# Performance work log

Measured on AMD Instinct MI355X. Metric: run time of the kernel, lower is better.

The kernel has to match this reference:

```python
import jax, jax.numpy as jnp
import numpy as np
import math

B, T, N, D = 8, 12, 500, 512  # batch, time(heads), nodes, K*d
FACTOR = 5
SAMPLE_K = min(FACTOR * math.ceil(math.log(N)), N)  # = 35, also n_top (N_Q == N_K)
W_SCALE = 0.02


def setup_inputs() -> dict:
    key = jax.random.key(0)
    ks = jax.random.split(key, 9)
    f32 = jnp.float32
    return {
        "X":   jax.random.normal(ks[0], (B, T, N, D), f32),
        "STE": jax.random.normal(ks[1], (B, T, N, D), f32),
        "Wq":  jax.random.normal(ks[2], (2 * D, D), f32) * W_SCALE,
        "bq":  jnp.zeros((D,), f32),
        "Wk":  jax.random.normal(ks[3], (2 * D, D), f32) * W_SCALE,
        "bk":  jnp.zeros((D,), f32),
        "Wv":  jax.random.normal(ks[4], (2 * D, D), f32) * W_SCALE,
        "bv":  jnp.zeros((D,), f32),
        "sample_idx": jax.random.randint(ks[5], (N, SAMPLE_K), 0, N, jnp.int32),
    }


def reference(X, STE, Wq, bq, Wk, bk, Wv, bv, sample_idx):
    # concat spatial features with spatio-temporal embedding -> projections
    Xc = jnp.concatenate([X, STE], axis=-1)                  # [B,T,N,2D]
    q = jax.nn.relu(Xc @ Wq + bq)                            # [B,T,N,D]
    k = jax.nn.relu(Xc @ Wk + bk)
    v = jax.nn.relu(Xc @ Wv + bv)

    n_top = SAMPLE_K
    # _prob_QK: sampled Q-K scores. Since SAMPLE_K*D >> N, computing the full
    # [B,T,N,N] score matrix and gathering the sampled columns is strictly
    # cheaper in memory than materializing K_sample [B,T,N,S,D] as torch does;
    # the math (Q_K_sample values) is identical.
    scores_full = jnp.einsum('bhld,bhmd->bhlm', q, k)        # [B,T,N,N]
    QK_sample = jnp.take_along_axis(
        scores_full, sample_idx[None, None, :, :], axis=3)   # [B,T,N,S]
    # sparsity measure M = max - mean (mean over L_K = N)
    M = QK_sample.max(axis=-1) - QK_sample.sum(axis=-1) / N  # [B,T,N]
    _, idx = jax.lax.top_k(M, n_top)                         # [B,T,n_top]

    # reduced-query full attention scores (gather rows of full scores == Q_reduce @ K^T)
    scores = jnp.take_along_axis(scores_full, idx[..., None], axis=2)  # [B,T,u,N]
    scores = scores * (1.0 / math.sqrt(D))

    # ProbMask (mask_flag=True): causal mask per selected query position
    j = jnp.arange(N)
    mask = j[None, None, None, :] > idx[..., None]           # [B,T,u,N]
    scores = jnp.where(mask, -jnp.inf, scores)
    attn = jax.nn.softmax(scores, axis=-1)                   # [B,T,u,N]
    ctx_new = jnp.einsum('bhun,bhnd->bhud', attn, v)         # [B,T,u,D]

    # initial context = causal cumsum of V, then scatter-update selected queries
    context = jnp.cumsum(v, axis=2)                          # [B,T,N,D]
    bi = jnp.arange(B)[:, None, None]
    hi = jnp.arange(T)[None, :, None]
    context = context.at[bi, hi, idx].set(ctx_new)
    # .transpose(2,1) in torch -> swap axes 1 and 2
    return context.transpose(0, 2, 1, 3)                     # [B,N,T,D]
```

## Files before the change

### kernel.cpp

```cpp
#include <hip/hip_runtime.h>
#include <math.h>

#define B_    8
#define T_    12
#define BT    96
#define NN    500
#define DD    512
#define KK    1024
#define SK    35
#define MROWS 48000

typedef __bf16 bf16x8 __attribute__((ext_vector_type(8)));
typedef float f32x4 __attribute__((ext_vector_type(4)));
typedef unsigned short u16;
typedef unsigned int u32;
typedef u16 ushort8_t __attribute__((ext_vector_type(8)));
typedef u16 ushort4_t __attribute__((ext_vector_type(4)));

__device__ __forceinline__ u16 bf_hi(float x) {
  __bf16 h = (__bf16)x;
  return __builtin_bit_cast(u16, h);
}
__device__ __forceinline__ float bf_tof(u16 b) {
  unsigned int u = ((unsigned int)b) << 16;
  return __builtin_bit_cast(float, u);
}

__device__ __forceinline__ int lds_off(int row, int kq) {
  return row * 32 + ((kq ^ ((row >> 1) & 3)) * 8);
}

__device__ __forceinline__ void gload_lds16(const u16* g, u16* l) {
  __builtin_amdgcn_global_load_lds(
      (const __attribute__((address_space(1))) u32*)g,
      (__attribute__((address_space(3))) u32*)l, 16, 0, 0);
}

__global__ __launch_bounds__(256) void convW_kernel(
    const float* __restrict__ W, u16* __restrict__ Bth, u16* __restrict__ Btl)
{
  const int n = blockIdx.x;
  const int k0 = threadIdx.x * 4;
  float xs[4];
#pragma unroll
  for (int j = 0; j < 4; ++j) xs[j] = W[(size_t)(k0 + j) * 512 + n];
  ushort4_t hi, lo;
#pragma unroll
  for (int j = 0; j < 4; ++j) {
    u16 h = bf_hi(xs[j]);
    hi[j] = h;
    lo[j] = bf_hi(xs[j] - bf_tof(h));
  }
  *(ushort4_t*)(Bth + (size_t)n * 1024 + k0) = hi;
  *(ushort4_t*)(Btl + (size_t)n * 1024 + k0) = lo;
}

template<int PASSES>
__global__ __launch_bounds__(256) void mfma_proj(
    const float* __restrict__ X, const float* __restrict__ STE,
    const u16* __restrict__ Bth, const u16* __restrict__ Btl,
    const float* __restrict__ bias, float* __restrict__ out)
{
  constexpr int NT = (PASSES == 3) ? 4 : 2;
  __shared__ u16 ldsbuf[2 * NT * 4096];
  const int tid = threadIdx.x;
  const int lane = tid & 63;
  const int wid = tid >> 6;
  const int wm = wid >> 1, wn = wid & 1;
  const int orig = blockIdx.x;
  const int xcd = orig & 7, pos = orig >> 3;
  const int wg = (xcd < 4 ? xcd * 188 : 752 + (xcd - 4) * 187) + pos;
  const int r0 = (wg >> 2) * 128;
  const int c0 = (wg & 3) * 128;
  const int fr = lane & 15, fk = lane >> 4;
  const int rin = lane >> 2;
  const int qq  = lane & 3;

  f32x4 acc[4][4];
#pragma unroll
  for (int m = 0; m < 4; ++m)
#pragma unroll
    for (int n = 0; n < 4; ++n) acc[m][n] = f32x4{0.f, 0.f, 0.f, 0.f};

  float4 a0[2], a1[2];

  auto LOAD_A = [&](int kt) {
    const int kk0 = kt * 32;
#pragma unroll
    for (int p = 0; p < 2; ++p) {
      const int c = tid + p * 256;
      const int row = c >> 2, kc = c & 3;
      const int col = kk0 + kc * 8;
      const float* src = (col < 512)
          ? (X + (size_t)(r0 + row) * 512 + col)
          : (STE + (size_t)(r0 + row) * 512 + (col - 512));
      a0[p] = *(const float4*)src;
      a1[p] = *(const float4*)(src + 4);
    }
  };
  auto ISSUE_B = [&](int buf, int kt) {
    u16* bBh = ldsbuf + buf * NT * 4096 + 4096;
    u16* bBl = ldsbuf + buf * NT * 4096 + 12288;
    const int kk0 = kt * 32;
#pragma unroll
    for (int i = 0; i < 2; ++i) {
      const int ch = wid * 2 + i;
      const int row = ch * 16 + rin;
      const int kq = qq ^ ((row >> 1) & 3);
      const size_t gb = (size_t)(c0 + row) * 1024 + kk0 + kq * 8;
      gload_lds16(Bth + gb, bBh + ch * 512);
      if (PASSES == 3) gload_lds16(Btl + gb, bBl + ch * 512);
    }
  };
  auto WRITE_A = [&](int buf) {
    u16* bAh = ldsbuf + buf * NT * 4096;
    u16* bAl = bAh + 8192;
#pragma unroll
    for (int p = 0; p < 2; ++p) {
      const int c = tid + p * 256;
      const int row = c >> 2, kc = c & 3;
      const int dst = lds_off(row, kc);
      float xs[8] = {a0[p].x, a0[p].y, a0[p].z, a0[p].w,
                     a1[p].x, a1[p].y, a1[p].z, a1[p].w};
      ushort8_t hi, lo;
#pragma unroll
      for (int j = 0; j < 8; ++j) {
        u16 h = bf_hi(xs[j]);
        hi[j] = h;
        if (PASSES == 3) lo[j] = bf_hi(xs[j] - bf_tof(h));
      }
      *(ushort8_t*)&bAh[dst] = hi;
      if (PASSES == 3) *(ushort8_t*)&bAl[dst] = lo;
    }
  };

  LOAD_A(0);
  ISSUE_B(0, 0);
  WRITE_A(0);
  __syncthreads();
  int cur = 0;

  for (int kt = 0; kt < 32; ++kt) {
    const bool more = (kt + 1 < 32);
    if (more) {
      LOAD_A(kt + 1);
      ISSUE_B(cur ^ 1, kt + 1);
    }
    u16* bAh = ldsbuf + cur * NT * 4096;
    u16* bBh = bAh + 4096;
    u16* bAl = bAh + 8192;
    u16* bBl = bAh + 12288;
    bf16x8 ah[4], al[4];
#pragma unroll
    for (int m = 0; m < 4; ++m) {
      const int off = lds_off(wm * 64 + m * 16 + fr, fk);
      ah[m] = *(const bf16x8*)&bAh[off];
      if (PASSES == 3) al[m] = *(const bf16x8*)&bAl[off];
    }
#pragma unroll
    for (int n = 0; n < 4; ++n) {
      const int off = lds_off(wn * 64 + n * 16 + fr, fk);
      bf16x8 bh = *(const bf16x8*)&bBh[off];
      bf16x8 bl;
      if (PASSES == 3) bl = *(const bf16x8*)&bBl[off];
#pragma unroll
      for (int m = 0; m < 4; ++m) {
        acc[m][n] = __builtin_amdgcn_mfma_f32_16x16x32_bf16(
            ah[m], bh, acc[m][n], 0, 0, 0);
        if (PASSES == 3) {
          acc[m][n] = __builtin_amdgcn_mfma_f32_16x16x32_bf16(
              ah[m], bl, acc[m][n], 0, 0, 0);
          acc[m][n] = __builtin_amdgcn_mfma_f32_16x16x32_bf16(
              al[m], bh, acc[m][n], 0, 0, 0);
        }
      }
    }
    if (more) WRITE_A(cur ^ 1);
    __syncthreads();
    cur ^= 1;
  }

#pragma unroll
  for (int n = 0; n < 4; ++n) {
    const int col = c0 + wn * 64 + n * 16 + fr;
    const float bb = bias[col];
#pragma unroll
    for (int m = 0; m < 4; ++m) {
      const int rowb = r0 + wm * 64 + m * 16 + fk * 4;
#pragma unroll
      for (int r = 0; r < 4; ++r)
        out[(size_t)(rowb + r) * 512 + col] = fmaxf(acc[m][n][r] + bb, 0.f);
    }
  }
}

__global__ __launch_bounds__(256) void sampled_M_kernel(
    const float* __restrict__ q, const float* __restrict__ k,
    const int* __restrict__ sidx, float* __restrict__ Mout)
{
  const int tid = threadIdx.x;
  const int lane = tid & 63, wid = tid >> 6;
  const int bid = blockIdx.x;
  const int xcd = bid & 7, j = bid >> 3;
  const int btg = j / 125, ub = j - btg * 125;
  const int bt = btg * 8 + xcd;
  __shared__ int sIdx[4][SK];
  if (tid < 4 * SK) {
    const int w = tid / SK, s = tid - w * SK;
    sIdx[w][s] = sidx[(ub * 4 + w) * SK + s];
  }
  __syncthreads();
  const int nn = ub * 4 + wid;
  const int n = bt * NN + nn;
  const float* qrow = q + (size_t)n * DD + lane * 8;
  float4 q0 = *(const float4*)qrow;
  float4 q1 = *(const float4*)(qrow + 4);
  const float* kbase = k + (size_t)bt * NN * DD + lane * 8;
  float mx = -INFINITY, sm = 0.f;
  for (int s0 = 0; s0 < SK; s0 += 5) {
    float p[5];
#pragma unroll
    for (int u = 0; u < 5; ++u) {
      const float* krow = kbase + (size_t)sIdx[wid][s0 + u] * DD;
      float4 k0 = *(const float4*)krow;
      float4 k1 = *(const float4*)(krow + 4);
      p[u] = q0.x*k0.x + q0.y*k0.y + q0.z*k0.z + q0.w*k0.w
           + q1.x*k1.x + q1.y*k1.y + q1.z*k1.z + q1.w*k1.w;
    }
#pragma unroll
    for (int off = 32; off > 0; off >>= 1)
#pragma unroll
      for (int u = 0; u < 5; ++u) p[u] += __shfl_xor(p[u], off);
#pragma unroll
    for (int u = 0; u < 5; ++u) { mx = fmaxf(mx, p[u]); sm += p[u]; }
  }
  if (lane == 0) Mout[n] = mx - sm * (1.0f / (float)NN);
}

__global__ __launch_bounds__(256) void topk_kernel(
    const float* __restrict__ Mb, int* __restrict__ idxb,
    int* __restrict__ sqi, int* __restrict__ su)
{
  const int bt = blockIdx.x;
  const int tid = threadIdx.x;
  __shared__ float mv[NN];
  __shared__ float rv[256];
  __shared__ int ri[256];
  __shared__ int qsel[SK];
  for (int n = tid; n < NN; n += 256) mv[n] = Mb[(size_t)bt * NN + n];
  __syncthreads();
  for (int it = 0; it < SK; ++it) {
    float bv = -INFINITY; int bi = NN;
    for (int n = tid; n < NN; n += 256) {
      float x = mv[n];
      if (x > bv) { bv = x; bi = n; }
    }
    rv[tid] = bv; ri[tid] = bi;
    __syncthreads();
    for (int sft = 128; sft > 0; sft >>= 1) {
      if (tid < sft) {
        float xv = rv[tid + sft]; int xi = ri[tid + sft];
        if (xv > rv[tid] || (xv == rv[tid] && xi < ri[tid])) {
          rv[tid] = xv; ri[tid] = xi;
        }
      }
      __syncthreads();
    }
    if (tid == 0) {
      idxb[bt * SK + it] = ri[0];
      qsel[it] = ri[0];
      mv[ri[0]] = -INFINITY;
    }
    __syncthreads();
  }
  if (tid < SK) {
    int myqi = qsel[tid];
    int rank = 0;
    for (int j = 0; j < SK; ++j) rank += (qsel[j] < myqi);
    sqi[bt * SK + rank] = myqi;
    su[bt * SK + rank] = tid;
  }
}

__global__ __launch_bounds__(256) void attn_part_kernel(
    const float* __restrict__ q, const float* __restrict__ k,
    const float* __restrict__ v, const int* __restrict__ sqi,
    float* __restrict__ pO, float* __restrict__ pm, float* __restrict__ pl)
{
  const int bid = blockIdx.x;
  const int xcd = bid & 7, j = bid >> 3;
  const int btg = j / 35, rem = j - btg * 35;
  const int g = rem / 5, c = rem % 5;
  const int bt = btg * 8 + xcd;
  const int base = bt * SK + g * 5;
  const int c0 = c * 100;
  const int tid = threadIdx.x;
  const int lane = tid & 63, wid = tid >> 6;

  __shared__ float sc[5][100];
  __shared__ int qg[5];
  __shared__ float pmx[5], psm[5];
  if (tid < 5) qg[tid] = sqi[base + tid];
  __syncthreads();
  const int gq = qg[4];
  const int mend = (gq < c0 + 99) ? gq : (c0 + 99);

  float4 qr[5][2];
#pragma unroll
  for (int jj = 0; jj < 5; ++jj) {
    const float* qp = q + ((size_t)bt * NN + qg[jj]) * DD + lane * 8;
    qr[jj][0] = *(const float4*)qp;
    qr[jj][1] = *(const float4*)(qp + 4);
  }
  const float scale = 0.044194173824159216f;

  for (int m = c0 + wid; m <= mend; m += 4) {
    const float* krow = k + ((size_t)bt * NN + m) * DD + lane * 8;
    float4 k0 = *(const float4*)krow;
    float4 k1 = *(const float4*)(krow + 4);
    float p[5];
#pragma unroll
    for (int jj = 0; jj < 5; ++jj) {
      p[jj] = qr[jj][0].x*k0.x + qr[jj][0].y*k0.y
            + qr[jj][0].z*k0.z + qr[jj][0].w*k0.w
            + qr[jj][1].x*k1.x + qr[jj][1].y*k1.y
            + qr[jj][1].z*k1.z + qr[jj][1].w*k1.w;
    }
#pragma unroll
    for (int off = 32; off > 0; off >>= 1)
#pragma unroll
      for (int jj = 0; jj < 5; ++jj) p[jj] += __shfl_xor(p[jj], off);
    if (lane == 0) {
#pragma unroll
      for (int jj = 0; jj < 5; ++jj) sc[jj][m - c0] = p[jj] * scale;
    }
  }
  __syncthreads();

  for (int jj = wid; jj < 5; jj += 4) {
    const int qe = (qg[jj] < c0 + 99) ? qg[jj] : (c0 + 99);
    const int len = qe - c0 + 1;
    float mx = -3e38f;
    for (int i = lane; i < len; i += 64) mx = fmaxf(mx, sc[jj][i]);
#pragma unroll
    for (int off = 32; off > 0; off >>= 1) mx = fmaxf(mx, __shfl_xor(mx, off));
    float sm = 0.f;
    for (int i = lane; i < len; i += 64) {
      float e = __expf(sc[jj][i] - mx);
      sc[jj][i] = e;
      sm += e;
    }
#pragma unroll
    for (int off = 32; off > 0; off >>= 1) sm += __shfl_xor(sm, off);
    if (lane == 0) { pmx[jj] = mx; psm[jj] = sm; }
  }
  __syncthreads();

  float a0[5] = {0.f,0.f,0.f,0.f,0.f}, a1[5] = {0.f,0.f,0.f,0.f,0.f};
  const float* vb = v + (size_t)bt * NN * DD;
  for (int m = c0; m <= mend; ++m) {
    float v0 = vb[(size_t)m * DD + tid];
    float v1 = vb[(size_t)m * DD + tid + 256];
#pragma unroll
    for (int jj = 0; jj < 5; ++jj) {
      if (m <= qg[jj]) {
        float w = sc[jj][m - c0];
        a0[jj] = fmaf(w, v0, a0[jj]);
        a1[jj] = fmaf(w, v1, a1[jj]);
      }
    }
  }

  const int pidx = (bt * 7 + g) * 5 + c;
  if (tid < 5) {
    pm[pidx * 5 + tid] = pmx[tid];
    pl[pidx * 5 + tid] = psm[tid];
  }
#pragma unroll
  for (int jj = 0; jj < 5; ++jj) {
    float* po = pO + ((size_t)(pidx * 5 + jj)) * DD;
    po[tid] = a0[jj];
    po[tid + 256] = a1[jj];
  }
}

__global__ __launch_bounds__(512) void attn_combine_kernel(
    const float* __restrict__ pO, const float* __restrict__ pm,
    const float* __restrict__ pl, const int* __restrict__ su,
    float* __restrict__ ctxn)
{
  const int bid = blockIdx.x;
  const int bt = bid / SK, s = bid % SK;
  const int g = s / 5, jj = s % 5;
  const int d = threadIdx.x;
  __shared__ float w[5];
  __shared__ float linv;
  if (d == 0) {
    float m_[5], l_[5], mx = -3e38f;
#pragma unroll
    for (int c = 0; c < 5; ++c) {
      const int pidx = (bt * 7 + g) * 5 + c;
      m_[c] = pm[pidx * 5 + jj];
      l_[c] = pl[pidx * 5 + jj];
      mx = fmaxf(mx, m_[c]);
    }
    float lt = 0.f;
#pragma unroll
    for (int c = 0; c < 5; ++c) {
      float wc = __expf(m_[c] - mx);
      w[c] = wc;
      lt += wc * l_[c];
    }
    linv = 1.f / lt;
  }
  __syncthreads();
  float o = 0.f;
#pragma unroll
  for (int c = 0; c < 5; ++c) {
    const int pidx = (bt * 7 + g) * 5 + c;
    o = fmaf(w[c], pO[((size_t)(pidx * 5 + jj)) * DD + d], o);
  }
  const int u = su[bt * SK + s];
  ctxn[((size_t)bt * SK + u) * DD + d] = o * linv;
}

__global__ __launch_bounds__(512) void vchunk_sum_kernel(
    const float* __restrict__ v, float* __restrict__ csum)
{
  const int ch = blockIdx.x, bt = blockIdx.y;
  const int d = threadIdx.x;
  const float* vb = v + ((size_t)bt * NN + ch * 50) * DD + d;
  float s = 0.f;
  for (int n = 0; n < 50; ++n) s += vb[(size_t)n * DD];
  csum[((size_t)bt * 10 + ch) * DD + d] = s;
}

__global__ __launch_bounds__(512) void cumsum_scatter2_kernel(
    const float* __restrict__ v, const int* __restrict__ idxb,
    const float* __restrict__ ctxn, const float* __restrict__ csum,
    float* __restrict__ out)
{
  const int ch = blockIdx.x, bt = blockIdx.y;
  const int b = bt / T_, t = bt % T_;
  const int d = threadIdx.x;
  const int n0 = ch * 50;
  __shared__ int sel[50];
  if (threadIdx.x < 50) sel[threadIdx.x] = -1;
  __syncthreads();
  if (threadIdx.x < SK) {
    int qi = idxb[bt * SK + threadIdx.x];
    if (qi >= n0 && qi < n0 + 50) sel[qi - n0] = threadIdx.x;
  }
  __syncthreads();
  float s = 0.f;
  for (int c = 0; c < ch; ++c) s += csum[((size_t)bt * 10 + c) * DD + d];
  for (int i = 0; i < 50; ++i) {
    s += v[((size_t)bt * NN + n0 + i) * DD + d];
    float o = s;
    int u = sel[i];
    if (u >= 0) o = ctxn[((size_t)bt * SK + u) * DD + d];
    out[(((size_t)b * NN + (n0 + i)) * T_ + t) * DD + d] = o;
  }
}

extern "C" void kernel_launch(void* const* d_in, const int* in_sizes, int n_in,
                              void* d_out, int out_size, void* d_ws, size_t ws_size,
                              hipStream_t stream) {
  const float* X   = (const float*)d_in[0];
  const float* STE = (const float*)d_in[1];
  const float* Wq  = (const float*)d_in[2];
  const float* bq  = (const float*)d_in[3];
  const float* Wk  = (const float*)d_in[4];
  const float* bk  = (const float*)d_in[5];
  const float* Wv  = (const float*)d_in[6];
  const float* bv  = (const float*)d_in[7];
  const int* sidx  = (const int*)d_in[8];
  float* out = (float*)d_out;

  float* q    = (float*)d_ws;
  float* k    = q + (size_t)MROWS * DD;
  float* v    = k + (size_t)MROWS * DD;
  float* Mb   = v + (size_t)MROWS * DD;
  int*   idxb = (int*)(Mb + MROWS);
  float* ctxn = (float*)(idxb + BT * SK);
  u16* Bqh = (u16*)(ctxn + (size_t)BT * SK * DD);
  u16* Bql = Bqh + (size_t)512 * 1024;
  u16* Bkh = Bql + (size_t)512 * 1024;
  u16* Bkl = Bkh + (size_t)512 * 1024;
  u16* Bvh = Bkl + (size_t)512 * 1024;
  u16* Bvl = Bvh + (size_t)512 * 1024;
  float* csum = (float*)Bqh;
  int*   sqi  = (int*)Bkh;
  int*   su   = sqi + BT * SK;
  float* pm   = (float*)(su + BT * SK);
  float* pl   = pm + 3360 * 5;
  float* pO   = (float*)d_out;
  (void)ws_size; (void)in_sizes; (void)n_in; (void)out_size;

  convW_kernel<<<512, 256, 0, stream>>>(Wq, Bqh, Bql);
  convW_kernel<<<512, 256, 0, stream>>>(Wk, Bkh, Bkl);
  convW_kernel<<<512, 256, 0, stream>>>(Wv, Bvh, Bvl);

  mfma_proj<3><<<1500, 256, 0, stream>>>(X, STE, Bqh, Bql, bq, q);
  mfma_proj<3><<<1500, 256, 0, stream>>>(X, STE, Bkh, Bkl, bk, k);
  mfma_proj<1><<<1500, 256, 0, stream>>>(X, STE, Bvh, Bvl, bv, v);

  sampled_M_kernel<<<12000, 256, 0, stream>>>(q, k, sidx, Mb);
  topk_kernel<<<BT, 256, 0, stream>>>(Mb, idxb, sqi, su);
  attn_part_kernel<<<3360, 256, 0, stream>>>(q, k, v, sqi, pO, pm, pl);
  attn_combine_kernel<<<3360, 512, 0, stream>>>(pO, pm, pl, su, ctxn);
  dim3 g5(10, BT);
  vchunk_sum_kernel<<<g5, 512, 0, stream>>>(v, csum);
  cumsum_scatter2_kernel<<<g5, 512, 0, stream>>>(v, idxb, ctxn, csum, out);
}
```

Baseline: 899.7 us.

## Load projection B operand directly from global into registers, bypassing LDS

The projection GEMM no longer stages the bf16 weight tiles (hi/lo) in shared memory through global_load_lds. Each wave now loads its B fragments straight from global memory into registers, double-buffered in registers, with the k-loop unrolled by two. This halves LDS usage and removes the LDS reads for B. In exchange it costs more VGPRs, and the B loads are redundant across the two wm waves and less coalesced, relying on L2/L1 hits.

```diff
diff --git a/kernel.cpp b/kernel.cpp
--- a/kernel.cpp
+++ b/kernel.cpp
@@ -30,12 +30,6 @@
   return row * 32 + ((kq ^ ((row >> 1) & 3)) * 8);
 }
 
-__device__ __forceinline__ void gload_lds16(const u16* g, u16* l) {
-  __builtin_amdgcn_global_load_lds(
-      (const __attribute__((address_space(1))) u32*)g,
-      (__attribute__((address_space(3))) u32*)l, 16, 0, 0);
-}
-
 __global__ __launch_bounds__(256) void convW_kernel(
     const float* __restrict__ W, u16* __restrict__ Bth, u16* __restrict__ Btl)
 {
@@ -61,8 +55,8 @@
     const u16* __restrict__ Bth, const u16* __restrict__ Btl,
     const float* __restrict__ bias, float* __restrict__ out)
 {
-  constexpr int NT = (PASSES == 3) ? 4 : 2;
-  __shared__ u16 ldsbuf[2 * NT * 4096];
+  constexpr int NA = (PASSES == 3) ? 2 : 1;
+  __shared__ u16 ldsA[2 * NA * 4096];
   const int tid = threadIdx.x;
   const int lane = tid & 63;
   const int wid = tid >> 6;
@@ -73,8 +67,6 @@
   const int r0 = (wg >> 2) * 128;
   const int c0 = (wg & 3) * 128;
   const int fr = lane & 15, fk = lane >> 4;
-  const int rin = lane >> 2;
-  const int qq  = lane & 3;
 
   f32x4 acc[4][4];
 #pragma unroll
@@ -82,7 +74,11 @@
 #pragma unroll
     for (int n = 0; n < 4; ++n) acc[m][n] = f32x4{0.f, 0.f, 0.f, 0.f};
 
+  const size_t bfo = (size_t)(c0 + wn * 64 + fr) * 1024 + fk * 8;
+
   float4 a0[2], a1[2];
+  bf16x8 bh0[4], bl0[4];
+  bf16x8 bh1[4], bl1[4];
 
   auto LOAD_A = [&](int kt) {
     const int kk0 = kt * 32;
@@ -98,23 +94,18 @@
       a1[p] = *(const float4*)(src + 4);
     }
   };
-  auto ISSUE_B = [&](int buf, int kt) {
-    u16* bBh = ldsbuf + buf * NT * 4096 + 4096;
-    u16* bBl = ldsbuf + buf * NT * 4096 + 12288;
-    const int kk0 = kt * 32;
-#pragma unroll
-    for (int i = 0; i < 2; ++i) {
-      const int ch = wid * 2 + i;
-      const int row = ch * 16 + rin;
-      const int kq = qq ^ ((row >> 1) & 3);
-      const size_t gb = (size_t)(c0 + row) * 1024 + kk0 + kq * 8;
-      gload_lds16(Bth + gb, bBh + ch * 512);
-      if (PASSES == 3) gload_lds16(Btl + gb, bBl + ch * 512);
+  auto LOAD_B = [&](int kt, bf16x8 (&h)[4], bf16x8 (&l)[4]) {
+    const int kk = kt * 32;
+#pragma unroll
+    for (int n = 0; n < 4; ++n) {
+      const size_t go = bfo + (size_t)n * 16384 + kk;
+      h[n] = *(const bf16x8*)(Bth + go);
+      if (PASSES == 3) l[n] = *(const bf16x8*)(Btl + go);
     }
   };
   auto WRITE_A = [&](int buf) {
-    u16* bAh = ldsbuf + buf * NT * 4096;
-    u16* bAl = bAh + 8192;
+    u16* bAh = ldsA + buf * NA * 4096;
+    u16* bAl = bAh + 4096;
 #pragma unroll
     for (int p = 0; p < 2; ++p) {
       const int c = tid + p * 256;
@@ -133,23 +124,9 @@
       if (PASSES == 3) *(ushort8_t*)&bAl[dst] = lo;
     }
   };
-
-  LOAD_A(0);
-  ISSUE_B(0, 0);
-  WRITE_A(0);
-  __syncthreads();
-  int cur = 0;
-
-  for (int kt = 0; kt < 32; ++kt) {
-    const bool more = (kt + 1 < 32);
-    if (more) {
-      LOAD_A(kt + 1);
-      ISSUE_B(cur ^ 1, kt + 1);
-    }
-    u16* bAh = ldsbuf + cur * NT * 4096;
-    u16* bBh = bAh + 4096;
-    u16* bAl = bAh + 8192;
-    u16* bBl = bAh + 12288;
+  auto COMPUTE = [&](int buf, const bf16x8 (&bh)[4], const bf16x8 (&bl)[4]) {
+    const u16* bAh = ldsA + buf * NA * 4096;
+    const u16* bAl = bAh + 4096;
     bf16x8 ah[4], al[4];
 #pragma unroll
     for (int m = 0; m < 4; ++m) {
@@ -158,26 +135,38 @@
       if (PASSES == 3) al[m] = *(const bf16x8*)&bAl[off];
     }
 #pragma unroll
-    for (int n = 0; n < 4; ++n) {
-      const int off = lds_off(wn * 64 + n * 16 + fr, fk);
-      bf16x8 bh = *(const bf16x8*)&bBh[off];
-      bf16x8 bl;
-      if (PASSES == 3) bl = *(const bf16x8*)&bBl[off];
+    for (int n = 0; n < 4; ++n)
 #pragma unroll
       for (int m = 0; m < 4; ++m) {
         acc[m][n] = __builtin_amdgcn_mfma_f32_16x16x32_bf16(
-            ah[m], bh, acc[m][n], 0, 0, 0);
+            ah[m], bh[n], acc[m][n], 0, 0, 0);
         if (PASSES == 3) {
           acc[m][n] = __builtin_amdgcn_mfma_f32_16x16x32_bf16(
-              ah[m], bl, acc[m][n], 0, 0, 0);
+              ah[m], bl[n], acc[m][n], 0, 0, 0);
           acc[m][n] = __builtin_amdgcn_mfma_f32_16x16x32_bf16(
-              al[m], bh, acc[m][n], 0, 0, 0);
+              al[m], bh[n], acc[m][n], 0, 0, 0);
         }
       }
-    }
-    if (more) WRITE_A(cur ^ 1);
+  };
+
+  LOAD_A(0);
+  LOAD_B(0, bh0, bl0);
+  WRITE_A(0);
+  __syncthreads();
+
+  for (int kt = 0; kt < 32; kt += 2) {
+    LOAD_A(kt + 1);
+    LOAD_B(kt + 1, bh1, bl1);
+    COMPUTE(0, bh0, bl0);
+    WRITE_A(1);
     __syncthreads();
-    cur ^= 1;
+    if (kt + 2 < 32) {
+      LOAD_A(kt + 2);
+      LOAD_B(kt + 2, bh0, bl0);
+    }
+    COMPUTE(1, bh1, bl1);
+    if (kt + 2 < 32) WRITE_A(0);
+    __syncthreads();
   }
 
 #pragma unroll
```

Result: slower. 1.062 ms (+18.1%).
